# Optimization experiments

Measured on AMD Instinct MI355X. Metric: run time of the kernel, lower is better.

Reference implementation:

```python
import jax, jax.numpy as jnp
import numpy as np

ND, NG, E = 25000, 20000, 1_000_000
DIN_D, DIN_G, H, OUT = 128, 128, 128, 128


def setup_inputs() -> dict:
    key = jax.random.key(0)
    ks = jax.random.split(key, 12)

    def w(k, i, o):
        return jax.random.normal(k, (i, o), jnp.float32) / np.float32(np.sqrt(i))

    return {
        "x_disease": jax.random.normal(ks[0], (ND, DIN_D), jnp.float32),
        "x_gene": jax.random.normal(ks[1], (NG, DIN_G), jnp.float32),
        "src": jax.random.randint(ks[2], (E,), 0, ND, dtype=jnp.int32),  # disease endpoint
        "dst": jax.random.randint(ks[3], (E,), 0, NG, dtype=jnp.int32),  # gene endpoint
        # layer 1, relation disease->gene: lin_l acts on aggregated disease feats, lin_r on gene feats
        "w1_dg_l": w(ks[4], DIN_D, H), "b1_dg": jnp.zeros((H,), jnp.float32), "w1_dg_r": w(ks[5], DIN_G, H),
        # layer 1, relation gene->disease (reverse edges)
        "w1_gd_l": w(ks[6], DIN_G, H), "b1_gd": jnp.zeros((H,), jnp.float32), "w1_gd_r": w(ks[7], DIN_D, H),
        # layer 2
        "w2_dg_l": w(ks[8], H, OUT), "b2_dg": jnp.zeros((OUT,), jnp.float32), "w2_dg_r": w(ks[9], H, OUT),
        "w2_gd_l": w(ks[10], H, OUT), "b2_gd": jnp.zeros((OUT,), jnp.float32), "w2_gd_r": w(ks[11], H, OUT),
    }


def _sage(x_src, x_dst, e_src, e_dst, n_dst, W_l, b_l, W_r):
    """Bipartite SAGEConv: lin_l(mean of source neighbors) + lin_r(x_dst)."""
    msg = x_src[e_src]                                         # [E, d] gather
    s = jax.ops.segment_sum(msg, e_dst, num_segments=n_dst)    # [n_dst, d]
    cnt = jax.ops.segment_sum(jnp.ones((e_dst.shape[0],), x_src.dtype),
                              e_dst, num_segments=n_dst)
    mean = s / jnp.maximum(cnt, 1.0)[:, None]                  # isolated nodes -> 0
    return mean @ W_l + b_l + x_dst @ W_r


def reference(x_disease, x_gene, src, dst,
              w1_dg_l, b1_dg, w1_dg_r, w1_gd_l, b1_gd, w1_gd_r,
              w2_dg_l, b2_dg, w2_dg_r, w2_gd_l, b2_gd, w2_gd_r):
    # HeteroConv aggr='sum': each node type receives from exactly one relation here,
    # so the cross-relation sum is the single relation output.
    g1 = _sage(x_disease, x_gene, src, dst, NG, w1_dg_l, b1_dg, w1_dg_r)   # gene <- disease
    d1 = _sage(x_gene, x_disease, dst, src, ND, w1_gd_l, b1_gd, w1_gd_r)   # disease <- gene (rev)
    g2 = _sage(d1, g1, src, dst, NG, w2_dg_l, b2_dg, w2_dg_r)
    d2 = _sage(g1, d1, dst, src, ND, w2_gd_l, b2_gd, w2_gd_r)
    return d2, g2
```

## Files before the change

### kernel.cpp

```cpp
#include <hip/hip_runtime.h>
#include <hip/hip_fp16.h>

#define ND 25000
#define NG 20000
#define NTOT (ND + NG)
#define NSCAN_BLOCKS 44
#define NBLK 128
#define PREPB 1024

typedef _Float16 half8 __attribute__((ext_vector_type(8)));
typedef float f32x4 __attribute__((ext_vector_type(4)));
typedef float f32x2 __attribute__((ext_vector_type(2)));

#define OFF_CNT    0ull
#define OFF_ROW    180224ull
#define OFF_BSUM   360448ull
#define OFF_PARTD  360704ull
#define OFF_PARTG  6760704ull
#define OFF_COL    11880704ull
#define OFF_WSW    15880704ull
#define OFF_XDH    16142848ull
#define OFF_XGH    22542848ull
#define OFF_X8D    27662848ull
#define OFF_X8G    30862848ull
#define OFF_MDH    33422848ull
#define OFF_MGH    39822848ull
#define OFF_D1H    44942848ull
#define OFF_G1H    51342848ull
#define OFF_D18    56462848ull
#define OFF_G18    59662848ull

struct WPtrs { const float* w[8]; };

__global__ __launch_bounds__(256) void prep_hist(const float* __restrict__ xd,
                                                 const float* __restrict__ xg,
                                                 __half* __restrict__ ydh,
                                                 __half* __restrict__ ygh,
                                                 unsigned char* __restrict__ y8d,
                                                 unsigned char* __restrict__ y8g,
                                                 WPtrs wp, _Float16* __restrict__ wsw,
                                                 const int* __restrict__ src,
                                                 const int* __restrict__ dst,
                                                 unsigned short* __restrict__ partD,
                                                 unsigned short* __restrict__ partG, int E) {
    __shared__ unsigned int h[12544];
    int bx = blockIdx.x, t = threadIdx.x;
    if (bx < 2 * NBLK) {
        bool isD = bx < NBLK;
        int bb = isD ? bx : bx - NBLK;
        const int* key = isD ? src : dst;
        int nw = isD ? (ND / 2) : (NG / 2);
        for (int i = t; i < nw; i += 256) h[i] = 0;
        __syncthreads();
        int e0 = (int)(((long long)E * bb) / NBLK);
        int e1 = (int)(((long long)E * (bb + 1)) / NBLK);
        for (int e = e0 + t; e < e1; e += 256) {
            int k = key[e];
            atomicAdd(&h[k >> 1], 1u << ((k & 1) * 16));
        }
        __syncthreads();
        unsigned int* po = (unsigned int*)((isD ? partD : partG) + (size_t)bb * (isD ? ND : NG));
        for (int i = t; i < nw; i += 256) po[i] = h[i];
        return;
    }
    int pb = bx - 2 * NBLK;
    if (pb < 8) {
        const float* W = wp.w[pb];
        _Float16* o = wsw + (size_t)pb * 16384;
        for (int rep = 0; rep < 8; ++rep) {
            int slot = rep * 256 + t;
            int lane = slot & 63, grp = slot >> 6;
            int kc = grp & 3, ntile = grp >> 2;
            int nn = ntile * 16 + (lane & 15);
            int kb = kc * 32 + (lane >> 4) * 8;
            half8 v;
#pragma unroll
            for (int j = 0; j < 8; ++j) v[j] = (_Float16)W[(size_t)(kb + j) * 128 + nn];
            *(half8*)(o + (size_t)slot * 8) = v;
        }
    }
    const int ndq = ND * 32;
    const int tot = ndq + NG * 32;
    for (int i = pb * 256 + t; i < tot; i += PREPB * 256) {
        const float* x;
        __half* y;
        unsigned char* y8;
        int idx;
        if (i < ndq) { x = xd; y = ydh; y8 = y8d; idx = i; }
        else         { x = xg; y = ygh; y8 = y8g; idx = i - ndq; }
        float4 v = ((const float4*)x)[idx];
        ((__half2*)y)[idx * 2 + 0] = __floats2half2_rn(v.x, v.y);
        ((__half2*)y)[idx * 2 + 1] = __floats2half2_rn(v.z, v.w);
        int p8 = __builtin_amdgcn_cvt_pk_fp8_f32(v.x, v.y, 0, false);
        p8 = __builtin_amdgcn_cvt_pk_fp8_f32(v.z, v.w, p8, true);
        ((int*)y8)[idx] = p8;
    }
}

__global__ __launch_bounds__(256) void colscan2(unsigned short* __restrict__ partD,
                                                unsigned short* __restrict__ partG,
                                                int* __restrict__ cnt) {
    int k = blockIdx.x * 256 + threadIdx.x;
    if (k >= NTOT) return;
    unsigned short* part;
    int nb, kk;
    if (k < ND) { part = partD; nb = ND; kk = k; }
    else        { part = partG; nb = NG; kk = k - ND; }
    int run = 0;
#pragma unroll 8
    for (int b = 0; b < NBLK; ++b) {
        size_t idx = (size_t)b * nb + kk;
        int v = part[idx];
        part[idx] = (unsigned short)run;
        run += v;
    }
    cnt[k] = run;
}

__global__ __launch_bounds__(256) void scan1(const int* __restrict__ cnt,
                                             int* __restrict__ row,
                                             int* __restrict__ bsum, int N) {
    __shared__ int sd[256];
    int t = threadIdx.x;
    int base = blockIdx.x * 1024 + t * 4;
    int v[4];
#pragma unroll
    for (int j = 0; j < 4; ++j) {
        int idx = base + j;
        v[j] = (idx < N) ? cnt[idx] : 0;
    }
    int tsum = v[0] + v[1] + v[2] + v[3];
    sd[t] = tsum;
    __syncthreads();
    for (int off = 1; off < 256; off <<= 1) {
        int x = (t >= off) ? sd[t - off] : 0;
        __syncthreads();
        sd[t] += x;
        __syncthreads();
    }
    int run = sd[t] - tsum;
#pragma unroll
    for (int j = 0; j < 4; ++j) {
        int idx = base + j;
        if (idx < N) row[idx] = run;
        run += v[j];
    }
    if (t == 255) bsum[blockIdx.x] = sd[255];
}

__global__ __launch_bounds__(256) void scan2(int* __restrict__ row,
                                             const int* __restrict__ bsum,
                                             int N, int total) {
    int off = 0;
    for (int b2 = 0; b2 < (int)blockIdx.x; ++b2) off += bsum[b2];
    int t = threadIdx.x;
    int base = blockIdx.x * 1024 + t * 4;
#pragma unroll
    for (int j = 0; j < 4; ++j) {
        int idx = base + j;
        if (idx < N) row[idx] += off;
    }
    if (blockIdx.x == 0 && t == 0) row[N] = total;
}

__global__ __launch_bounds__(256) void fill2(const int* __restrict__ src,
                                             const int* __restrict__ dst,
                                             const int* __restrict__ row,
                                             const unsigned short* __restrict__ partD,
                                             const unsigned short* __restrict__ partG,
                                             unsigned short* __restrict__ col, int E) {
    __shared__ unsigned int h[12544];
    int t = threadIdx.x, b = blockIdx.x;
    bool isD = b < NBLK;
    int bb = isD ? b : b - NBLK;
    const int* key = isD ? src : dst;
    const int* val = isD ? dst : src;
    const int* rowp = isD ? row : row + ND;
    int nw = isD ? (ND / 2) : (NG / 2);
    const unsigned int* pi =
        (const unsigned int*)((isD ? partD : partG) + (size_t)bb * (isD ? ND : NG));
    for (int i = t; i < nw; i += 256) h[i] = pi[i];
    __syncthreads();
    int e0 = (int)(((long long)E * bb) / NBLK);
    int e1 = (int)(((long long)E * (bb + 1)) / NBLK);
    for (int e = e0 + t; e < e1; e += 256) {
        int k = key[e];
        int v = val[e];
        unsigned int old = atomicAdd(&h[k >> 1], 1u << ((k & 1) * 16));
        int rank = (old >> ((k & 1) * 16)) & 0xffff;
        col[rowp[k] + rank] = (unsigned short)v;
    }
}

__global__ __launch_bounds__(256) void agg8m(const unsigned char* __restrict__ Xg,
                                             const unsigned char* __restrict__ Xd,
                                             const int* __restrict__ row,
                                             const unsigned short* __restrict__ col,
                                             __half* __restrict__ outd,
                                             __half* __restrict__ outg) {
    int wid = threadIdx.x >> 6, lane = threadIdx.x & 63;
    int node = blockIdx.x * 4 + wid;
    if (node >= NTOT) return;
    const unsigned char* X;
    _Float16* out;
    int nloc;
    if (node < ND) { X = Xg; out = (_Float16*)outd; nloc = node; }
    else           { X = Xd; out = (_Float16*)outg; nloc = node - ND; }
    int b = row[node], e = row[node + 1];
    int g = lane >> 3, f = lane & 7;
    float acc[16];
#pragma unroll
    for (int k = 0; k < 16; ++k) acc[k] = 0.f;
    int j = b + g;
    for (; j + 8 < e; j += 16) {
        int c0 = col[j], c1 = col[j + 8];
        int4 w0 = *(const int4*)(X + (size_t)c0 * 128 + f * 16);
        int4 w1 = *(const int4*)(X + (size_t)c1 * 128 + f * 16);
        const int* wa = (const int*)&w0;
        const int* wb = (const int*)&w1;
#pragma unroll
        for (int q = 0; q < 4; ++q) {
            f32x2 l0 = __builtin_amdgcn_cvt_pk_f32_fp8(wa[q], false);
            f32x2 h0 = __builtin_amdgcn_cvt_pk_f32_fp8(wa[q], true);
            f32x2 l1 = __builtin_amdgcn_cvt_pk_f32_fp8(wb[q], false);
            f32x2 h1 = __builtin_amdgcn_cvt_pk_f32_fp8(wb[q], true);
            acc[q * 4 + 0] += l0[0] + l1[0];
            acc[q * 4 + 1] += l0[1] + l1[1];
            acc[q * 4 + 2] += h0[0] + h1[0];
            acc[q * 4 + 3] += h0[1] + h1[1];
        }
    }
    if (j < e) {
        int c = col[j];
        int4 w = *(const int4*)(X + (size_t)c * 128 + f * 16);
        const int* wa = (const int*)&w;
#pragma unroll
        for (int q = 0; q < 4; ++q) {
            f32x2 l = __builtin_amdgcn_cvt_pk_f32_fp8(wa[q], false);
            f32x2 h = __builtin_amdgcn_cvt_pk_f32_fp8(wa[q], true);
            acc[q * 4 + 0] += l[0];
            acc[q * 4 + 1] += l[1];
            acc[q * 4 + 2] += h[0];
            acc[q * 4 + 3] += h[1];
        }
    }
#pragma unroll
    for (int k = 0; k < 16; ++k) {
        acc[k] += __shfl_xor(acc[k], 8, 64);
        acc[k] += __shfl_xor(acc[k], 16, 64);
        acc[k] += __shfl_xor(acc[k], 32, 64);
    }
    if (g == 0) {
        int deg = e - b;
        float r = 1.0f / (float)(deg > 0 ? deg : 1);
        half8 o0, o1;
#pragma unroll
        for (int k = 0; k < 8; ++k) o0[k] = (_Float16)(acc[k] * r);
#pragma unroll
        for (int k = 0; k < 8; ++k) o1[k] = (_Float16)(acc[8 + k] * r);
        _Float16* op = out + (size_t)nloc * 128 + f * 16;
        *(half8*)op = o0;
        *(half8*)(op + 8) = o1;
    }
}

struct GemmDual {
    const __half *A1d, *A2d, *A1g, *A2g;
    const _Float16 *W1d, *W2d, *W1g, *W2g;
    const float *biasd, *biasg;
    float *Yfd, *Yfg;
    __half *Yhd, *Yhg;
    unsigned char *Y8d, *Y8g;
};
__global__ __launch_bounds__(256) void gemm2(GemmDual p, int nblkD, int layer) {
    int bx = blockIdx.x;
    bool isD = bx < nblkD;
    const __half* A1 = isD ? p.A1d : p.A1g;
    const __half* A2 = isD ? p.A2d : p.A2g;
    const _Float16* W1 = isD ? p.W1d : p.W1g;
    const _Float16* W2 = isD ? p.W2d : p.W2g;
    const float* bias = isD ? p.biasd : p.biasg;
    float* Yf = isD ? p.Yfd : p.Yfg;
    __half* Yh = isD ? p.Yhd : p.Yhg;
    unsigned char* Y8 = isD ? p.Y8d : p.Y8g;
    int n = isD ? ND : NG, b0 = isD ? bx : bx - nblkD;
    int t = threadIdx.x;
    int wave = t >> 6, lane = t & 63;
    int row0 = b0 * 64 + wave * 16;
    if (row0 >= n) return;
    int m = lane & 15, quad = lane >> 4;
    int arow = row0 + m;
    if (arow >= n) arow = n - 1;
    const _Float16* a1p = (const _Float16*)A1 + (size_t)arow * 128 + quad * 8;
    const _Float16* a2p = (const _Float16*)A2 + (size_t)arow * 128 + quad * 8;
    half8 a1[4], a2[4];
#pragma unroll
    for (int kc = 0; kc < 4; ++kc) {
        a1[kc] = *(const half8*)(a1p + kc * 32);
        a2[kc] = *(const half8*)(a2p + kc * 32);
    }
#pragma unroll
    for (int ntile = 0; ntile < 8; ++ntile) {
        f32x4 acc = {0.f, 0.f, 0.f, 0.f};
#pragma unroll
        for (int kc = 0; kc < 4; ++kc) {
            half8 b1 = *(const half8*)(W1 + (size_t)((ntile * 4 + kc) * 64 + lane) * 8);
            acc = __builtin_amdgcn_mfma_f32_16x16x32_f16(a1[kc], b1, acc, 0, 0, 0);
            half8 b2 = *(const half8*)(W2 + (size_t)((ntile * 4 + kc) * 64 + lane) * 8);
            acc = __builtin_amdgcn_mfma_f32_16x16x32_f16(a2[kc], b2, acc, 0, 0, 0);
        }
        int colx = ntile * 16 + m;
        float bb = bias[colx];
#pragma unroll
        for (int r = 0; r < 4; ++r) {
            int rr = row0 + quad * 4 + r;
            if (rr < n) {
                float v = acc[r] + bb;
                if (layer == 2) {
                    Yf[(size_t)rr * 128 + colx] = v;
                } else {
                    Yh[(size_t)rr * 128 + colx] = __float2half(v);
                    int p8 = __builtin_amdgcn_cvt_pk_fp8_f32(v, v, 0, false);
                    Y8[(size_t)rr * 128 + colx] = (unsigned char)(p8 & 0xff);
                }
            }
        }
    }
}

extern "C" void kernel_launch(void* const* d_in, const int* in_sizes, int n_in,
                              void* d_out, int out_size, void* d_ws, size_t ws_size,
                              hipStream_t stream) {
    const float* x_d = (const float*)d_in[0];
    const float* x_g = (const float*)d_in[1];
    const int*   src = (const int*)d_in[2];
    const int*   dst = (const int*)d_in[3];
    float* out = (float*)d_out;

    char* ws = (char*)d_ws;
    int*            cnt   = (int*)(ws + OFF_CNT);
    int*            row   = (int*)(ws + OFF_ROW);
    int*            bsum  = (int*)(ws + OFF_BSUM);
    unsigned short* partD = (unsigned short*)(ws + OFF_PARTD);
    unsigned short* partG = (unsigned short*)(ws + OFF_PARTG);
    unsigned short* col   = (unsigned short*)(ws + OFF_COL);
    _Float16*       wsw   = (_Float16*)(ws + OFF_WSW);
    __half*         xd_h  = (__half*)(ws + OFF_XDH);
    __half*         xg_h  = (__half*)(ws + OFF_XGH);
    unsigned char*  x8d   = (unsigned char*)(ws + OFF_X8D);
    unsigned char*  x8g   = (unsigned char*)(ws + OFF_X8G);
    __half*         md_h  = (__half*)(ws + OFF_MDH);
    __half*         mg_h  = (__half*)(ws + OFF_MGH);
    __half*         d1_h  = (__half*)(ws + OFF_D1H);
    __half*         g1_h  = (__half*)(ws + OFF_G1H);
    unsigned char*  d1_8  = (unsigned char*)(ws + OFF_D18);
    unsigned char*  g1_8  = (unsigned char*)(ws + OFF_G18);

    const int E = in_sizes[2];
    const int nblkD = (ND + 63) / 64;
    const int nblkG = (NG + 63) / 64;

    WPtrs wp;
    wp.w[0] = (const float*)d_in[4];
    wp.w[1] = (const float*)d_in[6];
    wp.w[2] = (const float*)d_in[7];
    wp.w[3] = (const float*)d_in[9];
    wp.w[4] = (const float*)d_in[10];
    wp.w[5] = (const float*)d_in[12];
    wp.w[6] = (const float*)d_in[13];
    wp.w[7] = (const float*)d_in[15];
    const float* b1_dg = (const float*)d_in[5];
    const float* b1_gd = (const float*)d_in[8];
    const float* b2_dg = (const float*)d_in[11];
    const float* b2_gd = (const float*)d_in[14];

    prep_hist<<<2 * NBLK + PREPB, 256, 0, stream>>>(x_d, x_g, xd_h, xg_h, x8d, x8g,
                                                    wp, wsw, src, dst, partD, partG, E);
    colscan2<<<(NTOT + 255) / 256, 256, 0, stream>>>(partD, partG, cnt);
    scan1<<<NSCAN_BLOCKS, 256, 0, stream>>>(cnt, row, bsum, NTOT);
    scan2<<<NSCAN_BLOCKS, 256, 0, stream>>>(row, bsum, NTOT, 2 * E);
    fill2<<<2 * NBLK, 256, 0, stream>>>(src, dst, row, partD, partG, col, E);

    agg8m<<<(NTOT + 3) / 4, 256, 0, stream>>>(x8g, x8d, row, col, md_h, mg_h);
    GemmDual g1p;
    g1p.A1d = md_h; g1p.A2d = xd_h; g1p.W1d = wsw + 2 * 16384; g1p.W2d = wsw + 3 * 16384;
    g1p.biasd = b1_gd; g1p.Yfd = nullptr; g1p.Yhd = d1_h; g1p.Y8d = d1_8;
    g1p.A1g = mg_h; g1p.A2g = xg_h; g1p.W1g = wsw + 0 * 16384; g1p.W2g = wsw + 1 * 16384;
    g1p.biasg = b1_dg; g1p.Yfg = nullptr; g1p.Yhg = g1_h; g1p.Y8g = g1_8;
    gemm2<<<nblkD + nblkG, 256, 0, stream>>>(g1p, nblkD, 1);

    agg8m<<<(NTOT + 3) / 4, 256, 0, stream>>>(g1_8, d1_8, row, col, md_h, mg_h);
    GemmDual g2p;
    g2p.A1d = md_h; g2p.A2d = d1_h; g2p.W1d = wsw + 6 * 16384; g2p.W2d = wsw + 7 * 16384;
    g2p.biasd = b2_gd; g2p.Yfd = out; g2p.Yhd = nullptr; g2p.Y8d = nullptr;
    g2p.A1g = mg_h; g2p.A2g = g1_h; g2p.W1g = wsw + 4 * 16384; g2p.W2g = wsw + 5 * 16384;
    g2p.biasg = b2_dg; g2p.Yfg = out + (size_t)ND * 128; g2p.Yhg = nullptr; g2p.Y8g = nullptr;
    gemm2<<<nblkD + nblkG, 256, 0, stream>>>(g2p, nblkD, 2);
}
```

Before: 255.5 us.

## Fuse neighbor aggregation into GEMM and merge scan kernels with decoupled lookback

Merges the column scan and the two-pass prefix scan into a single kernel that publishes per-block aggregates through flags and spin-waits on predecessors. Fuses each mean-aggregation pass into the following dual GEMM: 512-thread blocks compute 64 node means into shared memory, then run MFMA from there. This drops the fp16 mean intermediate round-trip through global memory and removes four launches. The trade-offs are lower parallelism in the aggregation phase, since each wave now handles 8 nodes sequentially, and a spin-wait scan that relies on all 176 blocks being co-resident.

```diff
diff --git a/kernel.cpp b/kernel.cpp
--- a/kernel.cpp
+++ b/kernel.cpp
@@ -4,9 +4,9 @@
 #define ND 25000
 #define NG 20000
 #define NTOT (ND + NG)
-#define NSCAN_BLOCKS 44
 #define NBLK 128
 #define PREPB 1024
+#define NSB 176
 
 typedef _Float16 half8 __attribute__((ext_vector_type(8)));
 typedef float f32x4 __attribute__((ext_vector_type(4)));
@@ -23,8 +23,6 @@
 #define OFF_XGH    22542848ull
 #define OFF_X8D    27662848ull
 #define OFF_X8G    30862848ull
-#define OFF_MDH    33422848ull
-#define OFF_MGH    39822848ull
 #define OFF_D1H    44942848ull
 #define OFF_G1H    51342848ull
 #define OFF_D18    56462848ull
@@ -42,7 +40,8 @@
                                                  const int* __restrict__ src,
                                                  const int* __restrict__ dst,
                                                  unsigned short* __restrict__ partD,
-                                                 unsigned short* __restrict__ partG, int E) {
+                                                 unsigned short* __restrict__ partG,
+                                                 unsigned int* __restrict__ flags, int E) {
     __shared__ unsigned int h[12544];
     int bx = blockIdx.x, t = threadIdx.x;
     if (bx < 2 * NBLK) {
@@ -78,6 +77,8 @@
             for (int j = 0; j < 8; ++j) v[j] = (_Float16)W[(size_t)(kb + j) * 128 + nn];
             *(half8*)(o + (size_t)slot * 8) = v;
         }
+    } else if (pb == 8 && t < NSB) {
+        flags[t] = 0u;
     }
     const int ndq = ND * 32;
     const int tot = ndq + NG * 32;
@@ -97,39 +98,29 @@
     }
 }
 
-__global__ __launch_bounds__(256) void colscan2(unsigned short* __restrict__ partD,
-                                                unsigned short* __restrict__ partG,
-                                                int* __restrict__ cnt) {
-    int k = blockIdx.x * 256 + threadIdx.x;
-    if (k >= NTOT) return;
-    unsigned short* part;
-    int nb, kk;
-    if (k < ND) { part = partD; nb = ND; kk = k; }
-    else        { part = partG; nb = NG; kk = k - ND; }
+__global__ __launch_bounds__(256) void scanall(unsigned short* __restrict__ partD,
+                                               unsigned short* __restrict__ partG,
+                                               int* __restrict__ row,
+                                               unsigned int* __restrict__ flags, int E) {
+    __shared__ int sd[256];
+    __shared__ int sbase;
+    int t = threadIdx.x, bid = blockIdx.x;
+    int k = bid * 256 + t;
     int run = 0;
+    if (k < NTOT) {
+        unsigned short* part;
+        int nb, kk;
+        if (k < ND) { part = partD; nb = ND; kk = k; }
+        else        { part = partG; nb = NG; kk = k - ND; }
 #pragma unroll 8
-    for (int b = 0; b < NBLK; ++b) {
-        size_t idx = (size_t)b * nb + kk;
-        int v = part[idx];
-        part[idx] = (unsigned short)run;
-        run += v;
-    }
-    cnt[k] = run;
-}
-
-__global__ __launch_bounds__(256) void scan1(const int* __restrict__ cnt,
-                                             int* __restrict__ row,
-                                             int* __restrict__ bsum, int N) {
-    __shared__ int sd[256];
-    int t = threadIdx.x;
-    int base = blockIdx.x * 1024 + t * 4;
-    int v[4];
-#pragma unroll
-    for (int j = 0; j < 4; ++j) {
-        int idx = base + j;
-        v[j] = (idx < N) ? cnt[idx] : 0;
-    }
-    int tsum = v[0] + v[1] + v[2] + v[3];
+        for (int b = 0; b < NBLK; ++b) {
+            size_t idx = (size_t)b * nb + kk;
+            int v = part[idx];
+            part[idx] = (unsigned short)run;
+            run += v;
+        }
+    }
+    int tsum = run;
     sd[t] = tsum;
     __syncthreads();
     for (int off = 1; off < 256; off <<= 1) {
@@ -138,29 +129,27 @@
         sd[t] += x;
         __syncthreads();
     }
-    int run = sd[t] - tsum;
-#pragma unroll
-    for (int j = 0; j < 4; ++j) {
-        int idx = base + j;
-        if (idx < N) row[idx] = run;
-        run += v[j];
-    }
-    if (t == 255) bsum[blockIdx.x] = sd[255];
-}
-
-__global__ __launch_bounds__(256) void scan2(int* __restrict__ row,
-                                             const int* __restrict__ bsum,
-                                             int N, int total) {
-    int off = 0;
-    for (int b2 = 0; b2 < (int)blockIdx.x; ++b2) off += bsum[b2];
-    int t = threadIdx.x;
-    int base = blockIdx.x * 1024 + t * 4;
-#pragma unroll
-    for (int j = 0; j < 4; ++j) {
-        int idx = base + j;
-        if (idx < N) row[idx] += off;
-    }
-    if (blockIdx.x == 0 && t == 0) row[N] = total;
+    if (t == 0) {
+        unsigned int agg = (unsigned int)sd[255] + 1u;
+        __hip_atomic_store(&flags[bid], agg, __ATOMIC_RELEASE, __HIP_MEMORY_SCOPE_AGENT);
+    }
+    if (t < 64) {
+        int s = 0;
+        for (int i = t; i < bid; i += 64) {
+            unsigned int v;
+            do {
+                v = __hip_atomic_load(&flags[i], __ATOMIC_ACQUIRE, __HIP_MEMORY_SCOPE_AGENT);
+            } while (v == 0u);
+            s += (int)v - 1;
+        }
+#pragma unroll
+        for (int off = 1; off < 64; off <<= 1) s += __shfl_xor(s, off, 64);
+        if (t == 0) sbase = s;
+    }
+    __syncthreads();
+    int base = sbase;
+    if (k < NTOT) row[k] = base + sd[t] - tsum;
+    if (bid == 0 && t == 0) row[NTOT] = 2 * E;
 }
 
 __global__ __launch_bounds__(256) void fill2(const int* __restrict__ src,
@@ -192,90 +181,87 @@
     }
 }
 
-__global__ __launch_bounds__(256) void agg8m(const unsigned char* __restrict__ Xg,
-                                             const unsigned char* __restrict__ Xd,
-                                             const int* __restrict__ row,
-                                             const unsigned short* __restrict__ col,
-                                             __half* __restrict__ outd,
-                                             __half* __restrict__ outg) {
-    int wid = threadIdx.x >> 6, lane = threadIdx.x & 63;
-    int node = blockIdx.x * 4 + wid;
-    if (node >= NTOT) return;
-    const unsigned char* X;
-    _Float16* out;
-    int nloc;
-    if (node < ND) { X = Xg; out = (_Float16*)outd; nloc = node; }
-    else           { X = Xd; out = (_Float16*)outg; nloc = node - ND; }
-    int b = row[node], e = row[node + 1];
-    int g = lane >> 3, f = lane & 7;
-    float acc[16];
-#pragma unroll
-    for (int k = 0; k < 16; ++k) acc[k] = 0.f;
-    int j = b + g;
-    for (; j + 8 < e; j += 16) {
-        int c0 = col[j], c1 = col[j + 8];
-        int4 w0 = *(const int4*)(X + (size_t)c0 * 128 + f * 16);
-        int4 w1 = *(const int4*)(X + (size_t)c1 * 128 + f * 16);
-        const int* wa = (const int*)&w0;
-        const int* wb = (const int*)&w1;
-#pragma unroll
-        for (int q = 0; q < 4; ++q) {
-            f32x2 l0 = __builtin_amdgcn_cvt_pk_f32_fp8(wa[q], false);
-            f32x2 h0 = __builtin_amdgcn_cvt_pk_f32_fp8(wa[q], true);
-            f32x2 l1 = __builtin_amdgcn_cvt_pk_f32_fp8(wb[q], false);
-            f32x2 h1 = __builtin_amdgcn_cvt_pk_f32_fp8(wb[q], true);
-            acc[q * 4 + 0] += l0[0] + l1[0];
-            acc[q * 4 + 1] += l0[1] + l1[1];
-            acc[q * 4 + 2] += h0[0] + h1[0];
-            acc[q * 4 + 3] += h0[1] + h1[1];
-        }
-    }
-    if (j < e) {
-        int c = col[j];
-        int4 w = *(const int4*)(X + (size_t)c * 128 + f * 16);
-        const int* wa = (const int*)&w;
-#pragma unroll
-        for (int q = 0; q < 4; ++q) {
-            f32x2 l = __builtin_amdgcn_cvt_pk_f32_fp8(wa[q], false);
-            f32x2 h = __builtin_amdgcn_cvt_pk_f32_fp8(wa[q], true);
-            acc[q * 4 + 0] += l[0];
-            acc[q * 4 + 1] += l[1];
-            acc[q * 4 + 2] += h[0];
-            acc[q * 4 + 3] += h[1];
-        }
-    }
-#pragma unroll
-    for (int k = 0; k < 16; ++k) {
-        acc[k] += __shfl_xor(acc[k], 8, 64);
-        acc[k] += __shfl_xor(acc[k], 16, 64);
-        acc[k] += __shfl_xor(acc[k], 32, 64);
-    }
-    if (g == 0) {
-        int deg = e - b;
-        float r = 1.0f / (float)(deg > 0 ? deg : 1);
-        half8 o0, o1;
-#pragma unroll
-        for (int k = 0; k < 8; ++k) o0[k] = (_Float16)(acc[k] * r);
-#pragma unroll
-        for (int k = 0; k < 8; ++k) o1[k] = (_Float16)(acc[8 + k] * r);
-        _Float16* op = out + (size_t)nloc * 128 + f * 16;
-        *(half8*)op = o0;
-        *(half8*)(op + 8) = o1;
-    }
-}
-
-struct GemmDual {
-    const __half *A1d, *A2d, *A1g, *A2g;
+struct AggGemm {
+    const unsigned char *XtabD, *XtabG;
+    const __half *A2d, *A2g;
     const _Float16 *W1d, *W2d, *W1g, *W2g;
     const float *biasd, *biasg;
     float *Yfd, *Yfg;
     __half *Yhd, *Yhg;
     unsigned char *Y8d, *Y8g;
 };
-__global__ __launch_bounds__(256) void gemm2(GemmDual p, int nblkD, int layer) {
-    int bx = blockIdx.x;
+__global__ __launch_bounds__(512, 4) void aggemm(AggGemm p, const int* __restrict__ row,
+                                                 const unsigned short* __restrict__ col,
+                                                 int nblkD, int layer) {
+    __shared__ _Float16 smean[64][136];
+    int bx = blockIdx.x, t = threadIdx.x;
     bool isD = bx < nblkD;
-    const __half* A1 = isD ? p.A1d : p.A1g;
+    int n = isD ? ND : NG;
+    int b0 = isD ? bx : bx - nblkD;
+    int wv = t >> 6, lane = t & 63;
+    int g = lane >> 3, f = lane & 7;
+    const unsigned char* X = isD ? p.XtabD : p.XtabG;
+    for (int i = 0; i < 8; ++i) {
+        int loc = wv * 8 + i;
+        int nloc = b0 * 64 + loc;
+        if (nloc >= n) break;
+        int node = isD ? nloc : ND + nloc;
+        int b = row[node], e = row[node + 1];
+        float acc[16];
+#pragma unroll
+        for (int k = 0; k < 16; ++k) acc[k] = 0.f;
+        int j = b + g;
+        for (; j + 8 < e; j += 16) {
+            int c0 = col[j], c1 = col[j + 8];
+            int4 w0 = *(const int4*)(X + (size_t)c0 * 128 + f * 16);
+            int4 w1 = *(const int4*)(X + (size_t)c1 * 128 + f * 16);
+            const int* wa = (const int*)&w0;
+            const int* wb = (const int*)&w1;
+#pragma unroll
+            for (int q = 0; q < 4; ++q) {
+                f32x2 l0 = __builtin_amdgcn_cvt_pk_f32_fp8(wa[q], false);
+                f32x2 h0 = __builtin_amdgcn_cvt_pk_f32_fp8(wa[q], true);
+                f32x2 l1 = __builtin_amdgcn_cvt_pk_f32_fp8(wb[q], false);
+                f32x2 h1 = __builtin_amdgcn_cvt_pk_f32_fp8(wb[q], true);
+                acc[q * 4 + 0] += l0[0] + l1[0];
+                acc[q * 4 + 1] += l0[1] + l1[1];
+                acc[q * 4 + 2] += h0[0] + h1[0];
+                acc[q * 4 + 3] += h0[1] + h1[1];
+            }
+        }
+        if (j < e) {
+            int c = col[j];
+            int4 w = *(const int4*)(X + (size_t)c * 128 + f * 16);
+            const int* wa = (const int*)&w;
+#pragma unroll
+            for (int q = 0; q < 4; ++q) {
+                f32x2 l = __builtin_amdgcn_cvt_pk_f32_fp8(wa[q], false);
+                f32x2 h = __builtin_amdgcn_cvt_pk_f32_fp8(wa[q], true);
+                acc[q * 4 + 0] += l[0];
+                acc[q * 4 + 1] += l[1];
+                acc[q * 4 + 2] += h[0];
+                acc[q * 4 + 3] += h[1];
+            }
+        }
+#pragma unroll
+        for (int k = 0; k < 16; ++k) {
+            acc[k] += __shfl_xor(acc[k], 8, 64);
+            acc[k] += __shfl_xor(acc[k], 16, 64);
+            acc[k] += __shfl_xor(acc[k], 32, 64);
+        }
+        if (g == 0) {
+            int deg = e - b;
+            float r = 1.0f / (float)(deg > 0 ? deg : 1);
+            half8 o0, o1;
+#pragma unroll
+            for (int k = 0; k < 8; ++k) o0[k] = (_Float16)(acc[k] * r);
+#pragma unroll
+            for (int k = 0; k < 8; ++k) o1[k] = (_Float16)(acc[8 + k] * r);
+            *(half8*)&smean[loc][f * 16] = o0;
+            *(half8*)&smean[loc][f * 16 + 8] = o1;
+        }
+    }
+    __syncthreads();
     const __half* A2 = isD ? p.A2d : p.A2g;
     const _Float16* W1 = isD ? p.W1d : p.W1g;
     const _Float16* W2 = isD ? p.W2d : p.W2g;
@@ -283,31 +269,29 @@
     float* Yf = isD ? p.Yfd : p.Yfg;
     __half* Yh = isD ? p.Yhd : p.Yhg;
     unsigned char* Y8 = isD ? p.Y8d : p.Y8g;
-    int n = isD ? ND : NG, b0 = isD ? bx : bx - nblkD;
-    int t = threadIdx.x;
-    int wave = t >> 6, lane = t & 63;
-    int row0 = b0 * 64 + wave * 16;
-    if (row0 >= n) return;
+    int rgrp = wv >> 1;
+    int nt0 = (wv & 1) * 4;
+    int row0 = b0 * 64 + rgrp * 16;
     int m = lane & 15, quad = lane >> 4;
     int arow = row0 + m;
     if (arow >= n) arow = n - 1;
-    const _Float16* a1p = (const _Float16*)A1 + (size_t)arow * 128 + quad * 8;
     const _Float16* a2p = (const _Float16*)A2 + (size_t)arow * 128 + quad * 8;
     half8 a1[4], a2[4];
 #pragma unroll
     for (int kc = 0; kc < 4; ++kc) {
-        a1[kc] = *(const half8*)(a1p + kc * 32);
+        a1[kc] = *(const half8*)&smean[rgrp * 16 + m][quad * 8 + kc * 32];
         a2[kc] = *(const half8*)(a2p + kc * 32);
     }
 #pragma unroll
-    for (int ntile = 0; ntile < 8; ++ntile) {
-        f32x4 acc = {0.f, 0.f, 0.f, 0.f};
+    for (int nti = 0; nti < 4; ++nti) {
+        int ntile = nt0 + nti;
+        f32x4 acc4 = {0.f, 0.f, 0.f, 0.f};
 #pragma unroll
         for (int kc = 0; kc < 4; ++kc) {
             half8 b1 = *(const half8*)(W1 + (size_t)((ntile * 4 + kc) * 64 + lane) * 8);
-            acc = __builtin_amdgcn_mfma_f32_16x16x32_f16(a1[kc], b1, acc, 0, 0, 0);
+            acc4 = __builtin_amdgcn_mfma_f32_16x16x32_f16(a1[kc], b1, acc4, 0, 0, 0);
             half8 b2 = *(const half8*)(W2 + (size_t)((ntile * 4 + kc) * 64 + lane) * 8);
-            acc = __builtin_amdgcn_mfma_f32_16x16x32_f16(a2[kc], b2, acc, 0, 0, 0);
+            acc4 = __builtin_amdgcn_mfma_f32_16x16x32_f16(a2[kc], b2, acc4, 0, 0, 0);
         }
         int colx = ntile * 16 + m;
         float bb = bias[colx];
@@ -315,7 +299,7 @@
         for (int r = 0; r < 4; ++r) {
             int rr = row0 + quad * 4 + r;
             if (rr < n) {
-                float v = acc[r] + bb;
+                float v = acc4[r] + bb;
                 if (layer == 2) {
                     Yf[(size_t)rr * 128 + colx] = v;
                 } else {
@@ -338,9 +322,8 @@
     float* out = (float*)d_out;
 
     char* ws = (char*)d_ws;
-    int*            cnt   = (int*)(ws + OFF_CNT);
+    unsigned int*   flags = (unsigned int*)(ws + OFF_CNT);
     int*            row   = (int*)(ws + OFF_ROW);
-    int*            bsum  = (int*)(ws + OFF_BSUM);
     unsigned short* partD = (unsigned short*)(ws + OFF_PARTD);
     unsigned short* partG = (unsigned short*)(ws + OFF_PARTG);
     unsigned short* col   = (unsigned short*)(ws + OFF_COL);
@@ -349,8 +332,6 @@
     __half*         xg_h  = (__half*)(ws + OFF_XGH);
     unsigned char*  x8d   = (unsigned char*)(ws + OFF_X8D);
     unsigned char*  x8g   = (unsigned char*)(ws + OFF_X8G);
-    __half*         md_h  = (__half*)(ws + OFF_MDH);
-    __half*         mg_h  = (__half*)(ws + OFF_MGH);
     __half*         d1_h  = (__half*)(ws + OFF_D1H);
     __half*         g1_h  = (__half*)(ws + OFF_G1H);
     unsigned char*  d1_8  = (unsigned char*)(ws + OFF_D18);
@@ -375,25 +356,29 @@
     const float* b2_gd = (const float*)d_in[14];
 
     prep_hist<<<2 * NBLK + PREPB, 256, 0, stream>>>(x_d, x_g, xd_h, xg_h, x8d, x8g,
-                                                    wp, wsw, src, dst, partD, partG, E);
-    colscan2<<<(NTOT + 255) / 256, 256, 0, stream>>>(partD, partG, cnt);
-    scan1<<<NSCAN_BLOCKS, 256, 0, stream>>>(cnt, row, bsum, NTOT);
-    scan2<<<NSCAN_BLOCKS, 256, 0, stream>>>(row, bsum, NTOT, 2 * E);
+                                                    wp, wsw, src, dst, partD, partG, flags, E);
+    scanall<<<NSB, 256, 0, stream>>>(partD, partG, row, flags, E);
     fill2<<<2 * NBLK, 256, 0, stream>>>(src, dst, row, partD, partG, col, E);
 
-    agg8m<<<(NTOT + 3) / 4, 256, 0, stream>>>(x8g, x8d, row, col, md_h, mg_h);
-    GemmDual g1p;
-    g1p.A1d = md_h; g1p.A2d = xd_h; g1p.W1d = wsw + 2 * 16384; g1p.W2d = wsw + 3 * 16384;
-    g1p.biasd = b1_gd; g1p.Yfd = nullptr; g1p.Yhd = d1_h; g1p.Y8d = d1_8;
-    g1p.A1g = mg_h; g1p.A2g = xg_h; g1p.W1g = wsw + 0 * 16384; g1p.W2g = wsw + 1 * 16384;
-    g1p.biasg = b1_dg; g1p.Yfg = nullptr; g1p.Yhg = g1_h; g1p.Y8g = g1_8;
-    gemm2<<<nblkD + nblkG, 256, 0, stream>>>(g1p, nblkD, 1);
-
-    agg8m<<<(NTOT + 3) / 4, 256, 0, stream>>>(g1_8, d1_8, row, col, md_h, mg_h);
-    GemmDual g2p;
-    g2p.A1d = md_h; g2p.A2d = d1_h; g2p.W1d = wsw + 6 * 16384; g2p.W2d = wsw + 7 * 16384;
-    g2p.biasd = b2_gd; g2p.Yfd = out; g2p.Yhd = nullptr; g2p.Y8d = nullptr;
-    g2p.A1g = mg_h; g2p.A2g = g1_h; g2p.W1g = wsw + 4 * 16384; g2p.W2g = wsw + 5 * 16384;
-    g2p.biasg = b2_dg; g2p.Yfg = out + (size_t)ND * 128; g2p.Yhg = nullptr; g2p.Y8g = nullptr;
-    gemm2<<<nblkD + nblkG, 256, 0, stream>>>(g2p, nblkD, 2);
-}
+    AggGemm g1p;
+    g1p.XtabD = x8g; g1p.XtabG = x8d;
+    g1p.A2d = xd_h;  g1p.A2g = xg_h;
+    g1p.W1d = wsw + 2 * 16384; g1p.W2d = wsw + 3 * 16384;
+    g1p.W1g = wsw + 0 * 16384; g1p.W2g = wsw + 1 * 16384;
+    g1p.biasd = b1_gd; g1p.biasg = b1_dg;
+    g1p.Yfd = nullptr; g1p.Yfg = nullptr;
+    g1p.Yhd = d1_h; g1p.Y8d = d1_8;
+    g1p.Yhg = g1_h; g1p.Y8g = g1_8;
+    aggemm<<<nblkD + nblkG, 512, 0, stream>>>(g1p, row, col, nblkD, 1);
+
+    AggGemm g2p;
+    g2p.XtabD = g1_8; g2p.XtabG = d1_8;
+    g2p.A2d = d1_h;   g2p.A2g = g1_h;
+    g2p.W1d = wsw + 6 * 16384; g2p.W2d = wsw + 7 * 16384;
+    g2p.W1g = wsw + 4 * 16384; g2p.W2g = wsw + 5 * 16384;
+    g2p.biasd = b2_gd; g2p.biasg = b2_dg;
+    g2p.Yfd = out; g2p.Yfg = out + (size_t)ND * 128;
+    g2p.Yhd = nullptr; g2p.Y8d = nullptr;
+    g2p.Yhg = nullptr; g2p.Y8g = nullptr;
+    aggemm<<<nblkD + nblkG, 512, 0, stream>>>(g2p, row, col, nblkD, 2);
+}
```

Result: slower. 262.0 us (+2.6%).

## Fuse scan kernels with lookback prefix and map aggregation blocks per XCD

Applied to the files above, without the earlier changes.

Replaces the column scan plus two-pass block scan with a single kernel that passes block aggregates through flags in a decoupled-lookback style, removing two launches and the cnt/bsum round trips. Remaps agg8m blocks so half the XCDs handle disease nodes and half handle gene nodes, keeping each gathered feature table local to a subset of L2 caches. The lookback relies on all scan blocks being co-resident, and the new aggregation grid launches some idle blocks.

```diff
diff --git a/kernel.cpp b/kernel.cpp
--- a/kernel.cpp
+++ b/kernel.cpp
@@ -4,9 +4,11 @@
 #define ND 25000
 #define NG 20000
 #define NTOT (ND + NG)
-#define NSCAN_BLOCKS 44
 #define NBLK 128
 #define PREPB 1024
+#define NSB 176
+#define AGG_SLOTS 1563
+#define AGG_GRID (8 * AGG_SLOTS)
 
 typedef _Float16 half8 __attribute__((ext_vector_type(8)));
 typedef float f32x4 __attribute__((ext_vector_type(4)));
@@ -14,7 +16,6 @@
 
 #define OFF_CNT    0ull
 #define OFF_ROW    180224ull
-#define OFF_BSUM   360448ull
 #define OFF_PARTD  360704ull
 #define OFF_PARTG  6760704ull
 #define OFF_COL    11880704ull
@@ -42,7 +43,8 @@
                                                  const int* __restrict__ src,
                                                  const int* __restrict__ dst,
                                                  unsigned short* __restrict__ partD,
-                                                 unsigned short* __restrict__ partG, int E) {
+                                                 unsigned short* __restrict__ partG,
+                                                 unsigned int* __restrict__ flags, int E) {
     __shared__ unsigned int h[12544];
     int bx = blockIdx.x, t = threadIdx.x;
     if (bx < 2 * NBLK) {
@@ -78,6 +80,8 @@
             for (int j = 0; j < 8; ++j) v[j] = (_Float16)W[(size_t)(kb + j) * 128 + nn];
             *(half8*)(o + (size_t)slot * 8) = v;
         }
+    } else if (pb == 8 && t < NSB) {
+        flags[t] = 0u;
     }
     const int ndq = ND * 32;
     const int tot = ndq + NG * 32;
@@ -97,39 +101,29 @@
     }
 }
 
-__global__ __launch_bounds__(256) void colscan2(unsigned short* __restrict__ partD,
-                                                unsigned short* __restrict__ partG,
-                                                int* __restrict__ cnt) {
-    int k = blockIdx.x * 256 + threadIdx.x;
-    if (k >= NTOT) return;
-    unsigned short* part;
-    int nb, kk;
-    if (k < ND) { part = partD; nb = ND; kk = k; }
-    else        { part = partG; nb = NG; kk = k - ND; }
+__global__ __launch_bounds__(256) void scanall(unsigned short* __restrict__ partD,
+                                               unsigned short* __restrict__ partG,
+                                               int* __restrict__ row,
+                                               unsigned int* __restrict__ flags, int E) {
+    __shared__ int sd[256];
+    __shared__ int sbase;
+    int t = threadIdx.x, bid = blockIdx.x;
+    int k = bid * 256 + t;
     int run = 0;
+    if (k < NTOT) {
+        unsigned short* part;
+        int nb, kk;
+        if (k < ND) { part = partD; nb = ND; kk = k; }
+        else        { part = partG; nb = NG; kk = k - ND; }
 #pragma unroll 8
-    for (int b = 0; b < NBLK; ++b) {
-        size_t idx = (size_t)b * nb + kk;
-        int v = part[idx];
-        part[idx] = (unsigned short)run;
-        run += v;
-    }
-    cnt[k] = run;
-}
-
-__global__ __launch_bounds__(256) void scan1(const int* __restrict__ cnt,
-                                             int* __restrict__ row,
-                                             int* __restrict__ bsum, int N) {
-    __shared__ int sd[256];
-    int t = threadIdx.x;
-    int base = blockIdx.x * 1024 + t * 4;
-    int v[4];
-#pragma unroll
-    for (int j = 0; j < 4; ++j) {
-        int idx = base + j;
-        v[j] = (idx < N) ? cnt[idx] : 0;
-    }
-    int tsum = v[0] + v[1] + v[2] + v[3];
+        for (int b = 0; b < NBLK; ++b) {
+            size_t idx = (size_t)b * nb + kk;
+            int v = part[idx];
+            part[idx] = (unsigned short)run;
+            run += v;
+        }
+    }
+    int tsum = run;
     sd[t] = tsum;
     __syncthreads();
     for (int off = 1; off < 256; off <<= 1) {
@@ -138,29 +132,27 @@
         sd[t] += x;
         __syncthreads();
     }
-    int run = sd[t] - tsum;
-#pragma unroll
-    for (int j = 0; j < 4; ++j) {
-        int idx = base + j;
-        if (idx < N) row[idx] = run;
-        run += v[j];
-    }
-    if (t == 255) bsum[blockIdx.x] = sd[255];
-}
-
-__global__ __launch_bounds__(256) void scan2(int* __restrict__ row,
-                                             const int* __restrict__ bsum,
-                                             int N, int total) {
-    int off = 0;
-    for (int b2 = 0; b2 < (int)blockIdx.x; ++b2) off += bsum[b2];
-    int t = threadIdx.x;
-    int base = blockIdx.x * 1024 + t * 4;
-#pragma unroll
-    for (int j = 0; j < 4; ++j) {
-        int idx = base + j;
-        if (idx < N) row[idx] += off;
-    }
-    if (blockIdx.x == 0 && t == 0) row[N] = total;
+    if (t == 0) {
+        unsigned int agg = (unsigned int)sd[255] + 1u;
+        __hip_atomic_store(&flags[bid], agg, __ATOMIC_RELEASE, __HIP_MEMORY_SCOPE_AGENT);
+    }
+    if (t < 64) {
+        int s = 0;
+        for (int i = t; i < bid; i += 64) {
+            unsigned int v;
+            do {
+                v = __hip_atomic_load(&flags[i], __ATOMIC_ACQUIRE, __HIP_MEMORY_SCOPE_AGENT);
+            } while (v == 0u);
+            s += (int)v - 1;
+        }
+#pragma unroll
+        for (int off = 1; off < 64; off <<= 1) s += __shfl_xor(s, off, 64);
+        if (t == 0) sbase = s;
+    }
+    __syncthreads();
+    int base = sbase;
+    if (k < NTOT) row[k] = base + sd[t] - tsum;
+    if (bid == 0 && t == 0) row[NTOT] = 2 * E;
 }
 
 __global__ __launch_bounds__(256) void fill2(const int* __restrict__ src,
@@ -192,20 +184,30 @@
     }
 }
 
-__global__ __launch_bounds__(256) void agg8m(const unsigned char* __restrict__ Xg,
-                                             const unsigned char* __restrict__ Xd,
-                                             const int* __restrict__ row,
-                                             const unsigned short* __restrict__ col,
-                                             __half* __restrict__ outd,
-                                             __half* __restrict__ outg) {
+__global__ __launch_bounds__(256, 8) void agg8m(const unsigned char* __restrict__ Xg,
+                                                const unsigned char* __restrict__ Xd,
+                                                const int* __restrict__ row,
+                                                const unsigned short* __restrict__ col,
+                                                __half* __restrict__ outd,
+                                                __half* __restrict__ outg) {
     int wid = threadIdx.x >> 6, lane = threadIdx.x & 63;
-    int node = blockIdx.x * 4 + wid;
-    if (node >= NTOT) return;
+    int bid = blockIdx.x;
+    int xcd = bid & 7, slot = bid >> 3;
     const unsigned char* X;
     _Float16* out;
-    int nloc;
-    if (node < ND) { X = Xg; out = (_Float16*)outd; nloc = node; }
-    else           { X = Xd; out = (_Float16*)outg; nloc = node - ND; }
+    int node, nloc;
+    if (xcd < 4) {
+        int db = slot * 4 + xcd;
+        node = db * 4 + wid;
+        if (node >= ND) return;
+        X = Xg; out = (_Float16*)outd; nloc = node;
+    } else {
+        int gb = slot * 4 + (xcd - 4);
+        int gn = gb * 4 + wid;
+        if (gn >= NG) return;
+        node = ND + gn;
+        X = Xd; out = (_Float16*)outg; nloc = gn;
+    }
     int b = row[node], e = row[node + 1];
     int g = lane >> 3, f = lane & 7;
     float acc[16];
@@ -338,9 +340,8 @@
     float* out = (float*)d_out;
 
     char* ws = (char*)d_ws;
-    int*            cnt   = (int*)(ws + OFF_CNT);
+    unsigned int*   flags = (unsigned int*)(ws + OFF_CNT);
     int*            row   = (int*)(ws + OFF_ROW);
-    int*            bsum  = (int*)(ws + OFF_BSUM);
     unsigned short* partD = (unsigned short*)(ws + OFF_PARTD);
     unsigned short* partG = (unsigned short*)(ws + OFF_PARTG);
     unsigned short* col   = (unsigned short*)(ws + OFF_COL);
@@ -375,13 +376,11 @@
     const float* b2_gd = (const float*)d_in[14];
 
     prep_hist<<<2 * NBLK + PREPB, 256, 0, stream>>>(x_d, x_g, xd_h, xg_h, x8d, x8g,
-                                                    wp, wsw, src, dst, partD, partG, E);
-    colscan2<<<(NTOT + 255) / 256, 256, 0, stream>>>(partD, partG, cnt);
-    scan1<<<NSCAN_BLOCKS, 256, 0, stream>>>(cnt, row, bsum, NTOT);
-    scan2<<<NSCAN_BLOCKS, 256, 0, stream>>>(row, bsum, NTOT, 2 * E);
+                                                    wp, wsw, src, dst, partD, partG, flags, E);
+    scanall<<<NSB, 256, 0, stream>>>(partD, partG, row, flags, E);
     fill2<<<2 * NBLK, 256, 0, stream>>>(src, dst, row, partD, partG, col, E);
 
-    agg8m<<<(NTOT + 3) / 4, 256, 0, stream>>>(x8g, x8d, row, col, md_h, mg_h);
+    agg8m<<<AGG_GRID, 256, 0, stream>>>(x8g, x8d, row, col, md_h, mg_h);
     GemmDual g1p;
     g1p.A1d = md_h; g1p.A2d = xd_h; g1p.W1d = wsw + 2 * 16384; g1p.W2d = wsw + 3 * 16384;
     g1p.biasd = b1_gd; g1p.Yfd = nullptr; g1p.Yhd = d1_h; g1p.Y8d = d1_8;
@@ -389,7 +388,7 @@
     g1p.biasg = b1_dg; g1p.Yfg = nullptr; g1p.Yhg = g1_h; g1p.Y8g = g1_8;
     gemm2<<<nblkD + nblkG, 256, 0, stream>>>(g1p, nblkD, 1);
 
-    agg8m<<<(NTOT + 3) / 4, 256, 0, stream>>>(g1_8, d1_8, row, col, md_h, mg_h);
+    agg8m<<<AGG_GRID, 256, 0, stream>>>(g1_8, d1_8, row, col, md_h, mg_h);
     GemmDual g2p;
     g2p.A1d = md_h; g2p.A2d = d1_h; g2p.W1d = wsw + 6 * 16384; g2p.W2d = wsw + 7 * 16384;
     g2p.biasd = b2_gd; g2p.Yfd = out; g2p.Yhd = nullptr; g2p.Y8d = nullptr;
```

Measured after the change: 252.4 us. About the same (-1.2%).
